# Performance work log

Hardware: AMD Instinct MI355X
Metric: run time of the kernel (lower is better)

The kernel has to match this reference:

```python
import jax, jax.numpy as jnp
import numpy as np

D_MODEL = 1024
D_QK = 1024
NUM_HEADS = 16
HEAD_DIM = D_QK // NUM_HEADS      # 64
V_DIM = D_MODEL // NUM_HEADS      # 64
B, S = 2, 2048


def setup_inputs() -> dict:
    key = jax.random.key(0)
    ks = jax.random.split(key, 9)
    sc = 0.02
    return {
        "x": jax.random.normal(ks[0], (B, S, D_MODEL), dtype=jnp.float32),
        "Wqk": jax.random.normal(ks[1], (D_MODEL, 2 * D_QK), dtype=jnp.float32) * sc,
        "bqk": jax.random.normal(ks[2], (2 * D_QK,), dtype=jnp.float32) * sc,
        "Wv": jax.random.normal(ks[3], (D_MODEL, D_MODEL), dtype=jnp.float32) * sc,
        "bv": jax.random.normal(ks[4], (D_MODEL,), dtype=jnp.float32) * sc,
        "Wn": jax.random.normal(ks[5], (D_MODEL, NUM_HEADS), dtype=jnp.float32) * sc,
        "bn": jax.random.normal(ks[6], (NUM_HEADS,), dtype=jnp.float32) * sc,
        "Wo": jax.random.normal(ks[7], (D_MODEL, D_MODEL), dtype=jnp.float32) * sc,
        "bo": jax.random.normal(ks[8], (D_MODEL,), dtype=jnp.float32) * sc,
    }


def reference(x, Wqk, bqk, Wv, bv, Wn, bn, Wo, bo):
    b, s, _ = x.shape
    qk = x @ Wqk + bqk                                  # (B,S,2*D_QK)
    v = x @ Wv + bv                                     # (B,S,D_MODEL)
    n = x @ Wn + bn                                     # (B,S,H)

    qk = qk.reshape(b, s, 2, NUM_HEADS, HEAD_DIM)
    q, k = qk[:, :, 0], qk[:, :, 1]                     # (B,S,H,Dh)
    v = v.reshape(b, s, NUM_HEADS, V_DIM)               # (B,S,H,Dv)

    scores = jnp.einsum('bthd,bshd->bhts', q, k)        # (B,H,S,S)
    mask = jnp.tril(jnp.ones((s, s), dtype=scores.dtype))
    n_exp = jnp.exp(jnp.transpose(n, (0, 2, 1)))        # (B,H,S)
    attn = scores * mask / n_exp[:, :, :, None]         # dropout p=0 (eval)

    ctx = jnp.einsum('bhts,bshd->bthd', attn, v)        # (B,S,H,Dv)
    ctx = ctx.reshape(b, s, D_MODEL)
    return ctx @ Wo + bo
```

## Files before the change

### kernel.cpp

```cpp
#include <hip/hip_runtime.h>
#include <hip/hip_bf16.h>

constexpr int Bb   = 2;
constexpr int Ss   = 2048;
constexpr int Dm   = 1024;
constexpr int Hh   = 16;
constexpr int Hd   = 64;
constexpr int Mtot = Bb * Ss;
constexpr int NCH  = Ss / 64;

typedef __bf16 bf16x8 __attribute__((ext_vector_type(8)));
typedef float  f32x4  __attribute__((ext_vector_type(4)));
typedef __attribute__((address_space(1))) unsigned int u32_as1;
typedef __attribute__((address_space(3))) unsigned int u32_as3;

__device__ __forceinline__ void gload_lds16(const void* g, void* l) {
  __builtin_amdgcn_global_load_lds((const u32_as1*)g, (u32_as3*)l, 16, 0, 0);
}

__device__ __forceinline__ unsigned short f2bf(float f) {
  union { float f; unsigned u; } x; x.f = f;
  unsigned r = x.u + 0x7fffu + ((x.u >> 16) & 1u);
  return (unsigned short)(r >> 16);
}

__device__ __forceinline__ float bf2f(unsigned short s) {
  union { unsigned u; float f; } x; x.u = ((unsigned)s) << 16;
  return x.f;
}

__global__ void k_transpose_all(const float* __restrict__ W0, const float* __restrict__ W1,
                                const float* __restrict__ W2, unsigned short* __restrict__ D0,
                                unsigned short* __restrict__ D1, unsigned short* __restrict__ D2) {
  __shared__ float t[32][33];
  int z = blockIdx.z;
  int N = (z == 0) ? 2048 : 1024;
  int n0 = blockIdx.x * 32, k0 = blockIdx.y * 32;
  if (n0 >= N) return;
  const float* W = (z == 0) ? W0 : (z == 1) ? W1 : W2;
  unsigned short* Wt = (z == 0) ? D0 : (z == 1) ? D1 : D2;
  int tx = threadIdx.x, ty = threadIdx.y;
#pragma unroll
  for (int j = 0; j < 32; j += 8)
    t[ty + j][tx] = W[(size_t)(k0 + ty + j) * N + n0 + tx];
  __syncthreads();
#pragma unroll
  for (int j = 0; j < 32; j += 8)
    Wt[(size_t)(n0 + ty + j) * 1024 + k0 + tx] = f2bf(t[tx][ty + j]);
}

__global__ void k_n_proj(const float* __restrict__ x, const float* __restrict__ Wn,
                         const float* __restrict__ bn, float* __restrict__ invn,
                         unsigned short* __restrict__ xb) {
  __shared__ float xl[4][1024];
  int tid = threadIdx.x, w = tid >> 6, lane = tid & 63;
  int row = blockIdx.x * 4 + w;
  const float4* x4 = (const float4*)(x + (size_t)row * Dm);
  ushort4* xb4 = (ushort4*)(xb + (size_t)row * Dm);
#pragma unroll
  for (int j = 0; j < 4; ++j) {
    float4 v = x4[j * 64 + lane];
    *(float4*)&xl[w][(j * 64 + lane) * 4] = v;
    ushort4 o;
    o.x = f2bf(v.x); o.y = f2bf(v.y); o.z = f2bf(v.z); o.w = f2bf(v.w);
    xb4[j * 64 + lane] = o;
  }
  __syncthreads();
  const float4* Wn4 = (const float4*)Wn;
  f32x4 sum = {0.f, 0.f, 0.f, 0.f};
#pragma unroll 4
  for (int j = 0; j < 64; ++j) {
    float xv = xl[w][j * 16 + (lane >> 2)];
    float4 wv = Wn4[j * 64 + lane];
    sum[0] += xv * wv.x; sum[1] += xv * wv.y; sum[2] += xv * wv.z; sum[3] += xv * wv.w;
  }
#pragma unroll
  for (int m = 4; m < 64; m <<= 1) {
    sum[0] += __shfl_xor(sum[0], m);
    sum[1] += __shfl_xor(sum[1], m);
    sum[2] += __shfl_xor(sum[2], m);
    sum[3] += __shfl_xor(sum[3], m);
  }
  if (lane < 4) {
    int b = row >> 11, s = row & 2047;
#pragma unroll
    for (int e = 0; e < 4; ++e) {
      int h = lane * 4 + e;
      float nv = sum[e] + bn[h];
      invn[((size_t)(b * Hh + h)) * Ss + s] = expf(-nv);
    }
  }
}

__global__ __launch_bounds__(256, 4) void k_gemm_proj(
    const unsigned short* __restrict__ A, const unsigned short* __restrict__ BT,
    const float* __restrict__ bias0, const float* __restrict__ bias1,
    void* __restrict__ out0, void* __restrict__ out1, void* __restrict__ out2,
    void* __restrict__ out3, int M, int N, int K) {
  __shared__ __align__(16) unsigned short As[128 * 64];
  __shared__ __align__(16) unsigned short Bs[128 * 64];
  int tid = threadIdx.x, w = tid >> 6, lane = tid & 63;
  int m0 = blockIdx.y * 128, n0 = blockIdx.x * 128;
  int wm = w >> 1, wn = w & 1;
  f32x4 acc[4][4] = {};

  for (int kt = 0; kt < (K >> 6); ++kt) {
#pragma unroll
    for (int i = 0; i < 4; ++i) {
      int lin = i * 2048 + w * 512 + lane * 8;
      int r = lin >> 6, c = lin & 63;
      gload_lds16(A + (size_t)(m0 + r) * K + kt * 64 + c, As + i * 2048 + w * 512);
    }
#pragma unroll
    for (int i = 0; i < 4; ++i) {
      int lin = i * 2048 + w * 512 + lane * 8;
      int r = lin >> 6, c = lin & 63;
      gload_lds16(BT + (size_t)(n0 + r) * K + kt * 64 + c, Bs + i * 2048 + w * 512);
    }
    __syncthreads();
#pragma unroll
    for (int ks = 0; ks < 2; ++ks) {
      bf16x8 af[4], bfr[4];
#pragma unroll
      for (int mt = 0; mt < 4; ++mt)
        af[mt] = *(const bf16x8*)(As + (wm * 64 + mt * 16 + (lane & 15)) * 64 + ks * 32 + (lane >> 4) * 8);
#pragma unroll
      for (int nt = 0; nt < 4; ++nt)
        bfr[nt] = *(const bf16x8*)(Bs + (wn * 64 + nt * 16 + (lane & 15)) * 64 + ks * 32 + (lane >> 4) * 8);
#pragma unroll
      for (int mt = 0; mt < 4; ++mt)
#pragma unroll
        for (int nt = 0; nt < 4; ++nt)
          acc[mt][nt] = __builtin_amdgcn_mfma_f32_16x16x32_bf16(af[mt], bfr[nt], acc[mt][nt], 0, 0, 0);
    }
    __syncthreads();
  }

#pragma unroll
  for (int mt = 0; mt < 4; ++mt) {
#pragma unroll
    for (int nt = 0; nt < 4; ++nt) {
      int n = n0 + wn * 64 + nt * 16 + (lane & 15);
      int tbase = m0 + wm * 64 + mt * 16 + (lane >> 4) * 4;
      int region = n >> 10;
      int h = (n >> 6) & 15, d = n & 63;
      int b = tbase >> 11, t = tbase & 2047;
      float bb = (region < 2) ? bias0[n] : bias1[n - 2048];
      if (region == 0) {
        unsigned short* qp = (unsigned short*)out0;
#pragma unroll
        for (int r = 0; r < 4; ++r)
          qp[(((size_t)(b * Hh + h)) * Ss + t + r) * Hd + d] = f2bf(acc[mt][nt][r] + bb);
      } else if (region == 1) {
        unsigned short* kp = (unsigned short*)out1;
#pragma unroll
        for (int r = 0; r < 4; ++r)
          kp[(((size_t)(b * Hh + h)) * Ss + t + r) * Hd + d] = f2bf(acc[mt][nt][r] + bb);
        ushort4 o;
        o.x = f2bf(acc[mt][nt][0] + bb);
        o.y = f2bf(acc[mt][nt][1] + bb);
        o.z = f2bf(acc[mt][nt][2] + bb);
        o.w = f2bf(acc[mt][nt][3] + bb);
        *(ushort4*)((unsigned short*)out2 + ((size_t)(b * Hh + h) * Hd + d) * Ss + t) = o;
      } else {
        ushort4 o;
        o.x = f2bf(acc[mt][nt][0] + bb);
        o.y = f2bf(acc[mt][nt][1] + bb);
        o.z = f2bf(acc[mt][nt][2] + bb);
        o.w = f2bf(acc[mt][nt][3] + bb);
        *(ushort4*)((unsigned short*)out3 + ((size_t)(b * Hh + h) * Hd + d) * Ss + t) = o;
      }
    }
  }
}

__global__ __launch_bounds__(256, 5) void k_gemm_o(
    const unsigned short* __restrict__ A, const unsigned short* __restrict__ BT,
    const float* __restrict__ bias, float* __restrict__ out) {
  constexpr int K = 1024, N = 1024;
  __shared__ __align__(16) unsigned short As[64 * 64];
  __shared__ __align__(16) unsigned short Bs[128 * 64];
  int tid = threadIdx.x, w = tid >> 6, lane = tid & 63;
  int m0 = blockIdx.y * 64, n0 = blockIdx.x * 128;
  int wm = w >> 1, wn = w & 1;
  f32x4 acc[2][4] = {};

  for (int kt = 0; kt < (K >> 6); ++kt) {
#pragma unroll
    for (int i = 0; i < 2; ++i) {
      int lin = i * 2048 + w * 512 + lane * 8;
      int r = lin >> 6, c = lin & 63;
      gload_lds16(A + (size_t)(m0 + r) * K + kt * 64 + c, As + i * 2048 + w * 512);
    }
#pragma unroll
    for (int i = 0; i < 4; ++i) {
      int lin = i * 2048 + w * 512 + lane * 8;
      int r = lin >> 6, c = lin & 63;
      gload_lds16(BT + (size_t)(n0 + r) * K + kt * 64 + c, Bs + i * 2048 + w * 512);
    }
    __syncthreads();
#pragma unroll
    for (int ks = 0; ks < 2; ++ks) {
      bf16x8 af[2], bfr[4];
#pragma unroll
      for (int mt = 0; mt < 2; ++mt)
        af[mt] = *(const bf16x8*)(As + (wm * 32 + mt * 16 + (lane & 15)) * 64 + ks * 32 + (lane >> 4) * 8);
#pragma unroll
      for (int nt = 0; nt < 4; ++nt)
        bfr[nt] = *(const bf16x8*)(Bs + (wn * 64 + nt * 16 + (lane & 15)) * 64 + ks * 32 + (lane >> 4) * 8);
#pragma unroll
      for (int mt = 0; mt < 2; ++mt)
#pragma unroll
        for (int nt = 0; nt < 4; ++nt)
          acc[mt][nt] = __builtin_amdgcn_mfma_f32_16x16x32_bf16(af[mt], bfr[nt], acc[mt][nt], 0, 0, 0);
    }
    __syncthreads();
  }

#pragma unroll
  for (int mt = 0; mt < 2; ++mt) {
#pragma unroll
    for (int nt = 0; nt < 4; ++nt) {
      int n = n0 + wn * 64 + nt * 16 + (lane & 15);
      int m = m0 + wm * 32 + mt * 16 + (lane >> 4) * 4;
      float bb = bias[n];
#pragma unroll
      for (int r = 0; r < 4; ++r)
        out[(size_t)(m + r) * N + n] = acc[mt][nt][r] + bb;
    }
  }
}

__global__ __launch_bounds__(64) void k_gram(
    const unsigned short* __restrict__ vT, const unsigned short* __restrict__ kT,
    unsigned short* __restrict__ G) {
  int lane = threadIdx.x;
  int j = blockIdx.x, bh = blockIdx.y;
  int t0 = j * 64;
  const unsigned short* vb = vT + (size_t)bh * Hd * Ss;
  const unsigned short* kb = kT + (size_t)bh * Hd * Ss;
  unsigned short* g = G + ((size_t)bh * NCH + j) * 4096;

  bf16x8 af[4][2], bfr[4][2];
#pragma unroll
  for (int mt = 0; mt < 4; ++mt)
#pragma unroll
    for (int ks = 0; ks < 2; ++ks) {
      af[mt][ks]  = *(const bf16x8*)(vb + (size_t)(mt * 16 + (lane & 15)) * Ss + t0 + ks * 32 + (lane >> 4) * 8);
      bfr[mt][ks] = *(const bf16x8*)(kb + (size_t)(mt * 16 + (lane & 15)) * Ss + t0 + ks * 32 + (lane >> 4) * 8);
    }
  f32x4 acc[4][4] = {};
#pragma unroll
  for (int mt = 0; mt < 4; ++mt)
#pragma unroll
    for (int nt = 0; nt < 4; ++nt)
#pragma unroll
      for (int ks = 0; ks < 2; ++ks)
        acc[mt][nt] = __builtin_amdgcn_mfma_f32_16x16x32_bf16(af[mt][ks], bfr[nt][ks], acc[mt][nt], 0, 0, 0);
#pragma unroll
  for (int mt = 0; mt < 4; ++mt)
#pragma unroll
    for (int nt = 0; nt < 4; ++nt)
#pragma unroll
      for (int r = 0; r < 4; ++r)
        g[(mt * 16 + (lane >> 4) * 4 + r) * 64 + nt * 16 + (lane & 15)] = f2bf(acc[mt][nt][r]);
}

__global__ __launch_bounds__(256) void k_prefix(
    const unsigned short* __restrict__ G, unsigned short* __restrict__ Sp) {
  int gidx = blockIdx.x * 256 + threadIdx.x;
  int bh = gidx >> 12, e = gidx & 4095;
  const unsigned short* gp = G + (size_t)bh * NCH * 4096 + e;
  unsigned short* sp = Sp + (size_t)bh * NCH * 4096 + e;
  float acc = 0.f;
#pragma unroll 8
  for (int j = 0; j < NCH; ++j) {
    sp[(size_t)j * 4096] = f2bf(acc);
    acc += bf2f(gp[(size_t)j * 4096]);
  }
}

__global__ __launch_bounds__(256, 6) void k_chunk_attn(
    const unsigned short* __restrict__ q, const unsigned short* __restrict__ k,
    const unsigned short* __restrict__ vT, const unsigned short* __restrict__ Sp,
    const float* __restrict__ invn, unsigned short* __restrict__ ctx) {
  __shared__ __align__(16) unsigned short P[4 * 16 * 64];
  int tid = threadIdx.x, w = tid >> 6, lane = tid & 63;
  int j = blockIdx.x, bh = blockIdx.y;
  int t0 = j * 64;
  const unsigned short* qb = q + (size_t)bh * Ss * Hd;
  const unsigned short* kb = k + (size_t)bh * Ss * Hd;
  const unsigned short* vb = vT + (size_t)bh * Hd * Ss;
  const unsigned short* sp = Sp + ((size_t)bh * NCH + j) * 4096;

  bf16x8 qf[2];
#pragma unroll
  for (int ks = 0; ks < 2; ++ks)
    qf[ks] = *(const bf16x8*)(qb + (size_t)(t0 + w * 16 + (lane & 15)) * Hd + ks * 32 + (lane >> 4) * 8);

  f32x4 acc[4] = {};
#pragma unroll
  for (int nt = 0; nt < 4; ++nt)
#pragma unroll
    for (int ks = 0; ks < 2; ++ks) {
      bf16x8 sf = *(const bf16x8*)(sp + (nt * 16 + (lane & 15)) * 64 + ks * 32 + (lane >> 4) * 8);
      acc[nt] = __builtin_amdgcn_mfma_f32_16x16x32_bf16(qf[ks], sf, acc[nt], 0, 0, 0);
    }

  f32x4 sacc[4] = {};
#pragma unroll
  for (int nt = 0; nt < 4; ++nt)
#pragma unroll
    for (int ks = 0; ks < 2; ++ks) {
      bf16x8 kf = *(const bf16x8*)(kb + (size_t)(t0 + nt * 16 + (lane & 15)) * Hd + ks * 32 + (lane >> 4) * 8);
      sacc[nt] = __builtin_amdgcn_mfma_f32_16x16x32_bf16(qf[ks], kf, sacc[nt], 0, 0, 0);
    }

#pragma unroll
  for (int nt = 0; nt < 4; ++nt)
#pragma unroll
    for (int r = 0; r < 4; ++r) {
      int row = (lane >> 4) * 4 + r;
      int s_local = nt * 16 + (lane & 15);
      float vv = (s_local <= w * 16 + row) ? sacc[nt][r] : 0.f;
      int cb = s_local * 2;
      int byte = w * 2048 + row * 128 + (cb ^ ((row & 7) << 4));
      *(unsigned short*)((char*)P + byte) = f2bf(vv);
    }
  asm volatile("" ::: "memory");

  bf16x8 pf[2];
#pragma unroll
  for (int ks = 0; ks < 2; ++ks) {
    int prow = lane & 15;
    int pcb = (ks * 32 + (lane >> 4) * 8) * 2;
    pf[ks] = *(const bf16x8*)((char*)P + w * 2048 + prow * 128 + (pcb ^ ((prow & 7) << 4)));
  }
#pragma unroll
  for (int dt = 0; dt < 4; ++dt)
#pragma unroll
    for (int ks = 0; ks < 2; ++ks) {
      bf16x8 vf = *(const bf16x8*)(vb + (size_t)(dt * 16 + (lane & 15)) * Ss + t0 + ks * 32 + (lane >> 4) * 8);
      acc[dt] = __builtin_amdgcn_mfma_f32_16x16x32_bf16(pf[ks], vf, acc[dt], 0, 0, 0);
    }

  int b = bh >> 4, h = bh & 15;
  float sc[4];
#pragma unroll
  for (int r = 0; r < 4; ++r)
    sc[r] = invn[(size_t)bh * Ss + t0 + w * 16 + (lane >> 4) * 4 + r];
#pragma unroll
  for (int dt = 0; dt < 4; ++dt)
#pragma unroll
    for (int r = 0; r < 4; ++r) {
      int t = t0 + w * 16 + (lane >> 4) * 4 + r;
      size_t m = (size_t)b * Ss + t;
      ctx[m * Dm + h * Hd + dt * 16 + (lane & 15)] = f2bf(acc[dt][r] * sc[r]);
    }
}

extern "C" void kernel_launch(void* const* d_in, const int* in_sizes, int n_in,
                              void* d_out, int out_size, void* d_ws, size_t ws_size,
                              hipStream_t stream) {
  const float* x   = (const float*)d_in[0];
  const float* Wqk = (const float*)d_in[1];
  const float* bqk = (const float*)d_in[2];
  const float* Wv  = (const float*)d_in[3];
  const float* bv  = (const float*)d_in[4];
  const float* Wn  = (const float*)d_in[5];
  const float* bn  = (const float*)d_in[6];
  const float* Wo  = (const float*)d_in[7];
  const float* bo  = (const float*)d_in[8];

  char* ws = (char*)d_ws;
  size_t off = 0;
  unsigned short* xb    = (unsigned short*)(ws + off); off += (size_t)Mtot * Dm * 2;
  unsigned short* wprojT= (unsigned short*)(ws + off); off += (size_t)3072 * 1024 * 2;
  unsigned short* woT   = (unsigned short*)(ws + off); off += (size_t)1024 * 1024 * 2;
  unsigned short* qbuf  = (unsigned short*)(ws + off); off += (size_t)Bb * Hh * Ss * Hd * 2;
  unsigned short* kbuf  = (unsigned short*)(ws + off); off += (size_t)Bb * Hh * Ss * Hd * 2;
  unsigned short* ktbuf = (unsigned short*)(ws + off); off += (size_t)Bb * Hh * Ss * Hd * 2;
  unsigned short* vbuf  = (unsigned short*)(ws + off); off += (size_t)Bb * Hh * Ss * Hd * 2;
  float* invn           = (float*)(ws + off);          off += (size_t)Bb * Hh * Ss * 4;
  unsigned short* G     = (unsigned short*)(ws + off); off += (size_t)Bb * Hh * NCH * 4096 * 2;
  unsigned short* Sp    = (unsigned short*)(ws + off); off += (size_t)Bb * Hh * NCH * 4096 * 2;
  unsigned short* ctx   = xb;

  k_transpose_all<<<dim3(2048 / 32, 1024 / 32, 3), dim3(32, 8), 0, stream>>>(
      Wqk, Wv, Wo, wprojT, wprojT + (size_t)2048 * 1024, woT);

  k_n_proj<<<Mtot / 4, 256, 0, stream>>>(x, Wn, bn, invn, xb);

  k_gemm_proj<<<dim3(3072 / 128, Mtot / 128), 256, 0, stream>>>(
      xb, wprojT, bqk, bv, qbuf, kbuf, ktbuf, vbuf, Mtot, 3072, 1024);

  k_gram<<<dim3(NCH, Bb * Hh), 64, 0, stream>>>(vbuf, ktbuf, G);
  k_prefix<<<(Bb * Hh * 4096) / 256, 256, 0, stream>>>(G, Sp);
  k_chunk_attn<<<dim3(NCH, Bb * Hh), 256, 0, stream>>>(qbuf, kbuf, vbuf, Sp, invn, ctx);

  k_gemm_o<<<dim3(1024 / 128, Mtot / 64), 256, 0, stream>>>(ctx, woT, bo, (float*)d_out);
}
```

Measured before the change: 108.9 us.

## Fuse prep kernels, remap GEMM blocks per XCD, double-buffer output GEMM

The weight transpose and the n-projection/x-to-bf16 kernels are merged into one launch, with the block index choosing the role. This saves a launch and removes the previous grid's wasted blocks. Both GEMMs now remap block IDs so that consecutive M tiles land on the same XCD, which is meant to improve L2 reuse. The output GEMM gets double-buffered LDS with the next tile prefetched during compute, at the cost of more LDS and lower occupancy (launch bounds go from 5 to 3).

```diff
diff --git a/kernel.cpp b/kernel.cpp
--- a/kernel.cpp
+++ b/kernel.cpp
@@ -29,66 +29,75 @@
   return x.f;
 }
 
-__global__ void k_transpose_all(const float* __restrict__ W0, const float* __restrict__ W1,
-                                const float* __restrict__ W2, unsigned short* __restrict__ D0,
-                                unsigned short* __restrict__ D1, unsigned short* __restrict__ D2) {
-  __shared__ float t[32][33];
-  int z = blockIdx.z;
-  int N = (z == 0) ? 2048 : 1024;
-  int n0 = blockIdx.x * 32, k0 = blockIdx.y * 32;
-  if (n0 >= N) return;
-  const float* W = (z == 0) ? W0 : (z == 1) ? W1 : W2;
-  unsigned short* Wt = (z == 0) ? D0 : (z == 1) ? D1 : D2;
-  int tx = threadIdx.x, ty = threadIdx.y;
-#pragma unroll
-  for (int j = 0; j < 32; j += 8)
-    t[ty + j][tx] = W[(size_t)(k0 + ty + j) * N + n0 + tx];
-  __syncthreads();
-#pragma unroll
-  for (int j = 0; j < 32; j += 8)
-    Wt[(size_t)(n0 + ty + j) * 1024 + k0 + tx] = f2bf(t[tx][ty + j]);
-}
-
-__global__ void k_n_proj(const float* __restrict__ x, const float* __restrict__ Wn,
-                         const float* __restrict__ bn, float* __restrict__ invn,
-                         unsigned short* __restrict__ xb) {
-  __shared__ float xl[4][1024];
-  int tid = threadIdx.x, w = tid >> 6, lane = tid & 63;
-  int row = blockIdx.x * 4 + w;
-  const float4* x4 = (const float4*)(x + (size_t)row * Dm);
-  ushort4* xb4 = (ushort4*)(xb + (size_t)row * Dm);
-#pragma unroll
-  for (int j = 0; j < 4; ++j) {
-    float4 v = x4[j * 64 + lane];
-    *(float4*)&xl[w][(j * 64 + lane) * 4] = v;
-    ushort4 o;
-    o.x = f2bf(v.x); o.y = f2bf(v.y); o.z = f2bf(v.z); o.w = f2bf(v.w);
-    xb4[j * 64 + lane] = o;
-  }
-  __syncthreads();
-  const float4* Wn4 = (const float4*)Wn;
-  f32x4 sum = {0.f, 0.f, 0.f, 0.f};
+__global__ __launch_bounds__(256) void k_prep(
+    const float* __restrict__ x, const float* __restrict__ Wn, const float* __restrict__ bn,
+    float* __restrict__ invn, unsigned short* __restrict__ xb,
+    const float* __restrict__ Wqk, const float* __restrict__ Wv, const float* __restrict__ Wo,
+    unsigned short* __restrict__ wprojT, unsigned short* __restrict__ woT) {
+  __shared__ __align__(16) char smem[16384];
+  int bi = blockIdx.x;
+  int tid = threadIdx.x;
+  if (bi < 1024) {
+    float (*xl)[1024] = (float(*)[1024])smem;
+    int w = tid >> 6, lane = tid & 63;
+    int row = bi * 4 + w;
+    const float4* x4 = (const float4*)(x + (size_t)row * Dm);
+    ushort4* xb4 = (ushort4*)(xb + (size_t)row * Dm);
+#pragma unroll
+    for (int j = 0; j < 4; ++j) {
+      float4 v = x4[j * 64 + lane];
+      *(float4*)&xl[w][(j * 64 + lane) * 4] = v;
+      ushort4 o;
+      o.x = f2bf(v.x); o.y = f2bf(v.y); o.z = f2bf(v.z); o.w = f2bf(v.w);
+      xb4[j * 64 + lane] = o;
+    }
+    __syncthreads();
+    const float4* Wn4 = (const float4*)Wn;
+    f32x4 sum = {0.f, 0.f, 0.f, 0.f};
 #pragma unroll 4
-  for (int j = 0; j < 64; ++j) {
-    float xv = xl[w][j * 16 + (lane >> 2)];
-    float4 wv = Wn4[j * 64 + lane];
-    sum[0] += xv * wv.x; sum[1] += xv * wv.y; sum[2] += xv * wv.z; sum[3] += xv * wv.w;
-  }
-#pragma unroll
-  for (int m = 4; m < 64; m <<= 1) {
-    sum[0] += __shfl_xor(sum[0], m);
-    sum[1] += __shfl_xor(sum[1], m);
-    sum[2] += __shfl_xor(sum[2], m);
-    sum[3] += __shfl_xor(sum[3], m);
-  }
-  if (lane < 4) {
-    int b = row >> 11, s = row & 2047;
-#pragma unroll
-    for (int e = 0; e < 4; ++e) {
-      int h = lane * 4 + e;
-      float nv = sum[e] + bn[h];
-      invn[((size_t)(b * Hh + h)) * Ss + s] = expf(-nv);
-    }
+    for (int j = 0; j < 64; ++j) {
+      float xv = xl[w][j * 16 + (lane >> 2)];
+      float4 wv = Wn4[j * 64 + lane];
+      sum[0] += xv * wv.x; sum[1] += xv * wv.y; sum[2] += xv * wv.z; sum[3] += xv * wv.w;
+    }
+#pragma unroll
+    for (int m = 4; m < 64; m <<= 1) {
+      sum[0] += __shfl_xor(sum[0], m);
+      sum[1] += __shfl_xor(sum[1], m);
+      sum[2] += __shfl_xor(sum[2], m);
+      sum[3] += __shfl_xor(sum[3], m);
+    }
+    if (lane < 4) {
+      int b = row >> 11, s = row & 2047;
+#pragma unroll
+      for (int e = 0; e < 4; ++e) {
+        int h = lane * 4 + e;
+        float nv = sum[e] + bn[h];
+        invn[((size_t)(b * Hh + h)) * Ss + s] = expf(-nv);
+      }
+    }
+  } else {
+    float (*t)[33] = (float(*)[33])smem;
+    int ti = bi - 1024;
+    const float* W; unsigned short* Wt; int N, n0, k0;
+    if (ti < 2048) {
+      W = Wqk; Wt = wprojT; N = 2048;
+      n0 = (ti & 63) * 32; k0 = (ti >> 6) * 32;
+    } else if (ti < 3072) {
+      int l = ti - 2048; W = Wv; Wt = wprojT + (size_t)2048 * 1024; N = 1024;
+      n0 = (l & 31) * 32; k0 = (l >> 5) * 32;
+    } else {
+      int l = ti - 3072; W = Wo; Wt = woT; N = 1024;
+      n0 = (l & 31) * 32; k0 = (l >> 5) * 32;
+    }
+    int tx = tid & 31, ty = tid >> 5;
+#pragma unroll
+    for (int j = 0; j < 32; j += 8)
+      t[ty + j][tx] = W[(size_t)(k0 + ty + j) * N + n0 + tx];
+    __syncthreads();
+#pragma unroll
+    for (int j = 0; j < 32; j += 8)
+      Wt[(size_t)(n0 + ty + j) * 1024 + k0 + tx] = f2bf(t[tx][ty + j]);
   }
 }
 
@@ -100,7 +109,10 @@
   __shared__ __align__(16) unsigned short As[128 * 64];
   __shared__ __align__(16) unsigned short Bs[128 * 64];
   int tid = threadIdx.x, w = tid >> 6, lane = tid & 63;
-  int m0 = blockIdx.y * 128, n0 = blockIdx.x * 128;
+  int bid = blockIdx.y * gridDim.x + blockIdx.x;
+  int xcd = bid & 7, idx = bid >> 3;
+  int m0 = (xcd * 4 + (idx & 3)) * 128;
+  int n0 = (idx >> 2) * 128;
   int wm = w >> 1, wn = w & 1;
   f32x4 acc[4][4] = {};
 
@@ -174,40 +186,50 @@
   }
 }
 
-__global__ __launch_bounds__(256, 5) void k_gemm_o(
+__global__ __launch_bounds__(256, 3) void k_gemm_o(
     const unsigned short* __restrict__ A, const unsigned short* __restrict__ BT,
     const float* __restrict__ bias, float* __restrict__ out) {
   constexpr int K = 1024, N = 1024;
-  __shared__ __align__(16) unsigned short As[64 * 64];
-  __shared__ __align__(16) unsigned short Bs[128 * 64];
+  __shared__ __align__(16) unsigned short As[2][64 * 64];
+  __shared__ __align__(16) unsigned short Bs[2][128 * 64];
   int tid = threadIdx.x, w = tid >> 6, lane = tid & 63;
-  int m0 = blockIdx.y * 64, n0 = blockIdx.x * 128;
+  int bid = blockIdx.y * gridDim.x + blockIdx.x;
+  int xcd = bid & 7, idx = bid >> 3;
+  int m0 = (xcd * 8 + (idx & 7)) * 64;
+  int n0 = (idx >> 3) * 128;
   int wm = w >> 1, wn = w & 1;
   f32x4 acc[2][4] = {};
 
-  for (int kt = 0; kt < (K >> 6); ++kt) {
+  auto STAGE = [&](int kt, int cur) {
 #pragma unroll
     for (int i = 0; i < 2; ++i) {
       int lin = i * 2048 + w * 512 + lane * 8;
       int r = lin >> 6, c = lin & 63;
-      gload_lds16(A + (size_t)(m0 + r) * K + kt * 64 + c, As + i * 2048 + w * 512);
+      gload_lds16(A + (size_t)(m0 + r) * K + kt * 64 + c, As[cur] + i * 2048 + w * 512);
     }
 #pragma unroll
     for (int i = 0; i < 4; ++i) {
       int lin = i * 2048 + w * 512 + lane * 8;
       int r = lin >> 6, c = lin & 63;
-      gload_lds16(BT + (size_t)(n0 + r) * K + kt * 64 + c, Bs + i * 2048 + w * 512);
-    }
-    __syncthreads();
+      gload_lds16(BT + (size_t)(n0 + r) * K + kt * 64 + c, Bs[cur] + i * 2048 + w * 512);
+    }
+  };
+
+  constexpr int NT = K >> 6;
+  STAGE(0, 0);
+  __syncthreads();
+  for (int kt = 0; kt < NT; ++kt) {
+    int cur = kt & 1;
+    if (kt + 1 < NT) STAGE(kt + 1, cur ^ 1);
 #pragma unroll
     for (int ks = 0; ks < 2; ++ks) {
       bf16x8 af[2], bfr[4];
 #pragma unroll
       for (int mt = 0; mt < 2; ++mt)
-        af[mt] = *(const bf16x8*)(As + (wm * 32 + mt * 16 + (lane & 15)) * 64 + ks * 32 + (lane >> 4) * 8);
+        af[mt] = *(const bf16x8*)(As[cur] + (wm * 32 + mt * 16 + (lane & 15)) * 64 + ks * 32 + (lane >> 4) * 8);
 #pragma unroll
       for (int nt = 0; nt < 4; ++nt)
-        bfr[nt] = *(const bf16x8*)(Bs + (wn * 64 + nt * 16 + (lane & 15)) * 64 + ks * 32 + (lane >> 4) * 8);
+        bfr[nt] = *(const bf16x8*)(Bs[cur] + (wn * 64 + nt * 16 + (lane & 15)) * 64 + ks * 32 + (lane >> 4) * 8);
 #pragma unroll
       for (int mt = 0; mt < 2; ++mt)
 #pragma unroll
@@ -386,10 +408,7 @@
   unsigned short* Sp    = (unsigned short*)(ws + off); off += (size_t)Bb * Hh * NCH * 4096 * 2;
   unsigned short* ctx   = xb;
 
-  k_transpose_all<<<dim3(2048 / 32, 1024 / 32, 3), dim3(32, 8), 0, stream>>>(
-      Wqk, Wv, Wo, wprojT, wprojT + (size_t)2048 * 1024, woT);
-
-  k_n_proj<<<Mtot / 4, 256, 0, stream>>>(x, Wn, bn, invn, xb);
+  k_prep<<<5120, 256, 0, stream>>>(x, Wn, bn, invn, xb, Wqk, Wv, Wo, wprojT, woT);
 
   k_gemm_proj<<<dim3(3072 / 128, Mtot / 128), 256, 0, stream>>>(
       xb, wprojT, bqk, bv, qbuf, kbuf, ktbuf, vbuf, Mtot, 3072, 1024);
```

New measurement: 104.0 us. 4.5% less time.
